# Performance work log

Hardware: AMD Instinct MI355X
Metric: run time of the kernel (lower is better)

Reference implementation:

```python
import jax, jax.numpy as jnp
import numpy as np
import math

B, S, HID = 4, 2048, 2048
H, KV, D = 16, 4, 128  # heads, kv heads, head_dim; n_rep = H//KV = 4
THETA = 1000000.0


def setup_inputs() -> dict:
    key = jax.random.key(0)
    ks = jax.random.split(key, 6)
    x = jax.random.normal(ks[0], (B, S, HID), dtype=jnp.float32)
    # real RoPE tables (theta=1e6), shape [S, D]
    inv_freq = 1.0 / (THETA ** (jnp.arange(0, D, 2, dtype=jnp.float32) / D))
    t = jnp.arange(S, dtype=jnp.float32)
    freqs = jnp.outer(t, inv_freq)                      # [S, D/2]
    emb = jnp.concatenate([freqs, freqs], axis=-1)      # [S, D]
    cos, sin = jnp.cos(emb), jnp.sin(emb)
    scale = 0.02
    wq = jax.random.normal(ks[1], (H * D, HID), dtype=jnp.float32) * scale
    wk = jax.random.normal(ks[2], (KV * D, HID), dtype=jnp.float32) * scale
    wv = jax.random.normal(ks[3], (KV * D, HID), dtype=jnp.float32) * scale
    wo = jax.random.normal(ks[4], (HID, H * D), dtype=jnp.float32) * scale
    return {"x": x, "cos": cos, "sin": sin, "wq": wq, "wk": wk, "wv": wv, "wo": wo}


def _rotate_half(t):
    half = t.shape[-1] // 2
    return jnp.concatenate([-t[..., half:], t[..., :half]], axis=-1)


def reference(x, cos, sin, wq, wk, wv, wo):
    b, s, _ = x.shape
    rep = H // KV
    # QKV projections (torch Linear: y = x @ W^T)
    q = (x @ wq.T).reshape(b, s, H, D)
    k = (x @ wk.T).reshape(b, s, KV, D)
    v = (x @ wv.T).reshape(b, s, KV, D)
    # RoPE, cos/sin broadcast over batch and heads: [1, S, 1, D]
    c = cos[None, :s, None, :]
    si = sin[None, :s, None, :]
    q = q * c + _rotate_half(q) * si
    k = k * c + _rotate_half(k) * si
    # GQA without materializing repeated KV: group q heads as [KV, rep]
    qg = q.reshape(b, s, KV, rep, D)
    scale = 1.0 / math.sqrt(D)
    # flash path in source: SDPA with default is_causal=False -> full (non-causal) attention
    scores = jnp.einsum('bqkrd,bskd->bkrqs', qg, k) * scale  # [B, KV, rep, S, S]
    attn = jax.nn.softmax(scores, axis=-1)
    out = jnp.einsum('bkrqs,bskd->bqkrd', attn, v).reshape(b, s, H * D)
    return out @ wo.T
```

## Files before the change

### kernel.cpp

```cpp
#include <hip/hip_runtime.h>
#include <stdint.h>

#define BB 4
#define SS 2048
#define HIDW 2048
#define NH 16
#define NKV 4
#define DD 128

typedef unsigned short u16;
typedef __attribute__((ext_vector_type(8))) short bf16x8;
typedef __attribute__((ext_vector_type(4))) float f32x4;
typedef __attribute__((ext_vector_type(2))) float f32x2;
typedef __attribute__((ext_vector_type(2))) __bf16 bf16x2;

__device__ __forceinline__ u16 f2bf1(float f) {
  __bf16 h = (__bf16)f;
  return __builtin_bit_cast(u16, h);
}

__device__ __forceinline__ unsigned pkbf(float a, float b) {
  f32x2 v = {a, b};
  bf16x2 h = __builtin_convertvector(v, bf16x2);
  return __builtin_bit_cast(unsigned, h);
}

__device__ __forceinline__ void gld_lds16(const void* g, void* s) {
  __builtin_amdgcn_global_load_lds(
      (const __attribute__((address_space(1))) void*)g,
      (__attribute__((address_space(3))) void*)(unsigned)(uintptr_t)s,
      16, 0, 0);
}

__global__ __launch_bounds__(256) void cast_f32_bf16(const float* __restrict__ in,
                                                     u16* __restrict__ out, int n4) {
  int i = blockIdx.x * 256 + threadIdx.x;
  if (i < n4) {
    float4 f = ((const float4*)in)[i];
    uint2 o;
    o.x = pkbf(f.x, f.y);
    o.y = pkbf(f.z, f.w);
    ((uint2*)out)[i] = o;
  }
}

__global__ __launch_bounds__(256) void gemm_bt(const u16* __restrict__ A,
                                               const u16* __restrict__ Bt,
                                               float* __restrict__ C,
                                               int M, int N, int K) {
  __shared__ u16 As[128 * 32];
  __shared__ u16 Bs[128 * 32];
  const int tid = threadIdx.x;
  const int wave = tid >> 6, lane = tid & 63;
  const int lr = lane & 15, lq = lane >> 4;
  const int row0 = blockIdx.y * 128, col0 = blockIdx.x * 128;
  const int wm = (wave >> 1) * 64, wn = (wave & 1) * 64;

  const int trow = tid >> 2;
  const int tblk = (tid & 3) ^ (trow & 3);
  const u16* aSrc = A + (size_t)(row0 + trow) * K + tblk * 8;
  const u16* bSrc = Bt + (size_t)(col0 + trow) * K + tblk * 8;
  char* ldsA = (char*)As + wave * 1024;
  char* ldsB = (char*)Bs + wave * 1024;

  f32x4 acc[4][4] = {};
  const int aoff = (wm + lr) * 32 + ((lq ^ (lr & 3)) * 8);
  const int boff = (wn + lr) * 32 + ((lq ^ (lr & 3)) * 8);

  for (int k0 = 0; k0 < K; k0 += 32) {
    __syncthreads();
    gld_lds16(aSrc + k0, ldsA);
    gld_lds16(aSrc + (size_t)64 * K + k0, ldsA + 4096);
    gld_lds16(bSrc + k0, ldsB);
    gld_lds16(bSrc + (size_t)64 * K + k0, ldsB + 4096);
    __syncthreads();
    bf16x8 a[4], b[4];
#pragma unroll
    for (int i = 0; i < 4; i++) a[i] = *(const bf16x8*)(As + aoff + i * 512);
#pragma unroll
    for (int j = 0; j < 4; j++) b[j] = *(const bf16x8*)(Bs + boff + j * 512);
#pragma unroll
    for (int i = 0; i < 4; i++)
#pragma unroll
      for (int j = 0; j < 4; j++)
        acc[i][j] = __builtin_amdgcn_mfma_f32_16x16x32_bf16(a[i], b[j], acc[i][j], 0, 0, 0);
  }
#pragma unroll
  for (int i = 0; i < 4; i++) {
    int row = row0 + wm + i * 16 + lq * 4;
#pragma unroll
    for (int j = 0; j < 4; j++) {
      int col = col0 + wn + j * 16 + lr;
      float* cp = C + (size_t)row * N + col;
#pragma unroll
      for (int r = 0; r < 4; r++) cp[(size_t)r * N] = acc[i][j][r];
    }
  }
}

__global__ __launch_bounds__(256) void rope_qk(const float* __restrict__ qkv,
                                               const float* __restrict__ cosT,
                                               const float* __restrict__ sinT,
                                               u16* __restrict__ qb, u16* __restrict__ kb) {
  const float qscale = 0.08838834764831845f;
  int tok = blockIdx.x;
  int b = tok >> 11, s = tok & (SS - 1);
  for (int p = threadIdx.x; p < (NH + NKV) * 64; p += 256) {
    int head = p >> 6, dd = p & 63;
    float c0 = cosT[s * DD + dd];
    float c1 = cosT[s * DD + dd + 64];
    float s0 = sinT[s * DD + dd];
    float s1 = sinT[s * DD + dd + 64];
    if (head < NH) {
      const float* src = qkv + (size_t)tok * 3072 + head * DD;
      float x0 = src[dd], x1 = src[dd + 64];
      u16* dst = qb + ((size_t)(b * NH + head) * SS + s) * DD;
      dst[dd] = f2bf1((x0 * c0 - x1 * s0) * qscale);
      dst[dd + 64] = f2bf1((x1 * c1 + x0 * s1) * qscale);
    } else {
      int kv = head - NH;
      const float* src = qkv + (size_t)tok * 3072 + 2048 + kv * DD;
      float x0 = src[dd], x1 = src[dd + 64];
      u16* dst = kb + ((size_t)(b * NKV + kv) * SS + s) * DD;
      dst[dd] = f2bf1(x0 * c0 - x1 * s0);
      dst[dd + 64] = f2bf1(x1 * c1 + x0 * s1);
    }
  }
}

__global__ __launch_bounds__(256) void v_trans(const float* __restrict__ qkv,
                                               u16* __restrict__ vt) {
  __shared__ float tile[64][65];
  int bk = blockIdx.x;
  int b = bk >> 2, kv = bk & 3;
  int s0 = blockIdx.y * 64, d0 = blockIdx.z * 64;
  int t = threadIdx.x;
  int sl = t >> 2, dc = (t & 3) * 16;
  const float* src = qkv + ((size_t)(b * SS + s0 + sl)) * 3072 + 2560 + kv * DD + d0 + dc;
#pragma unroll
  for (int u = 0; u < 16; u += 4) {
    float4 v4 = *(const float4*)(src + u);
    tile[sl][dc + u] = v4.x; tile[sl][dc + u + 1] = v4.y;
    tile[sl][dc + u + 2] = v4.z; tile[sl][dc + u + 3] = v4.w;
  }
  __syncthreads();
  int dl = t >> 2, sc = (t & 3) * 16;
  u16* dst = vt + ((size_t)bk * DD + d0 + dl) * SS + s0 + sc;
#pragma unroll
  for (int u = 0; u < 16; u++) dst[u] = f2bf1(tile[sc + u][dl]);
}

__global__ __launch_bounds__(256, 2) void flash_attn(const u16* __restrict__ qb,
                                                     const u16* __restrict__ kb,
                                                     const u16* __restrict__ vt,
                                                     u16* __restrict__ ob) {
  __shared__ u16 Ks[64 * 128];
  __shared__ u16 Vs[128 * 64];
  __shared__ u16 Pt[128 * 64];
  const int tid = threadIdx.x;
  const int wave = tid >> 6, lane = tid & 63;
  const int lr = lane & 15, lq = lane >> 4;
  const int q0 = blockIdx.x * 128;
  const int bh = blockIdx.y;
  const int b = bh >> 4, h = bh & 15;
  const int kvh = h >> 2;
  const size_t kbase = (size_t)(b * NKV + kvh) * SS * DD;
  const size_t vbase = (size_t)(b * NKV + kvh) * DD * SS;

  bf16x8 qf[2][4];
#pragma unroll
  for (int nt = 0; nt < 2; nt++) {
    const u16* qrow = qb + ((size_t)bh * SS + q0 + wave * 32 + nt * 16 + lr) * DD + lq * 8;
#pragma unroll
    for (int kk = 0; kk < 4; kk++) qf[nt][kk] = *(const bf16x8*)(qrow + kk * 32);
  }

  f32x4 o_acc[8][2] = {};
  float l_i[2] = {0.0f, 0.0f};

  const int ktrow = tid >> 4;
  const int ktblk = (tid & 15) ^ ktrow;
  const u16* ksrc = kb + kbase + (size_t)ktrow * DD + ktblk * 8;
  const int vtrow = tid >> 3;
  const int vtblk = (tid & 7) ^ (vtrow & 7);
  const u16* vsrc = vt + vbase + (size_t)vtrow * SS + vtblk * 8;
  char* kdst = (char*)Ks + wave * 1024;
  char* vdst = (char*)Vs + wave * 1024;

  for (int s0 = 0; s0 < SS; s0 += 64) {
    __syncthreads();
#pragma unroll
    for (int c = 0; c < 4; c++)
      gld_lds16(ksrc + (size_t)(s0 + c * 16) * DD, kdst + c * 4096);
#pragma unroll
    for (int c = 0; c < 4; c++)
      gld_lds16(vsrc + s0 + (size_t)c * 32 * SS, vdst + c * 4096);
    __syncthreads();

    f32x4 sc[4][2] = {};
#pragma unroll
    for (int kk = 0; kk < 4; kk++) {
#pragma unroll
      for (int mt = 0; mt < 4; mt++) {
        bf16x8 kf = *(const bf16x8*)(Ks + (mt * 16 + lr) * 128 + (((kk * 4 + lq) ^ lr) * 8));
#pragma unroll
        for (int nt = 0; nt < 2; nt++)
          sc[mt][nt] = __builtin_amdgcn_mfma_f32_16x16x32_bf16(kf, qf[nt][kk], sc[mt][nt], 0, 0, 0);
      }
    }

#pragma unroll
    for (int nt = 0; nt < 2; nt++) {
      float rs = 0.0f;
#pragma unroll
      for (int mt = 0; mt < 4; mt++)
#pragma unroll
        for (int r = 0; r < 4; r++) {
          float p = __expf(sc[mt][nt][r]);
          sc[mt][nt][r] = p;
          rs += p;
        }
      l_i[nt] += rs;
      int prow = wave * 32 + nt * 16 + lr;
#pragma unroll
      for (int mt = 0; mt < 4; mt++) {
        uint2 pk;
        pk.x = pkbf(sc[mt][nt][0], sc[mt][nt][1]);
        pk.y = pkbf(sc[mt][nt][2], sc[mt][nt][3]);
        int bb = (mt * 2 + (lq >> 1)) ^ (lr & 7);
        *(uint2*)((char*)Pt + prow * 128 + bb * 16 + (lq & 1) * 8) = pk;
      }
    }

#pragma unroll
    for (int kk2 = 0; kk2 < 2; kk2++) {
      bf16x8 pbf[2];
#pragma unroll
      for (int nt = 0; nt < 2; nt++) {
        int prow = wave * 32 + nt * 16 + lr;
        pbf[nt] = *(const bf16x8*)((char*)Pt + prow * 128 + (((kk2 * 4 + lq) ^ (lr & 7)) * 16));
      }
#pragma unroll
      for (int mt = 0; mt < 8; mt++) {
        bf16x8 vf = *(const bf16x8*)(Vs + (mt * 16 + lr) * 64 + (((kk2 * 4 + lq) ^ (lr & 7)) * 8));
#pragma unroll
        for (int nt = 0; nt < 2; nt++)
          o_acc[mt][nt] = __builtin_amdgcn_mfma_f32_16x16x32_bf16(vf, pbf[nt], o_acc[mt][nt], 0, 0, 0);
      }
    }
  }

#pragma unroll
  for (int nt = 0; nt < 2; nt++) {
    float l = l_i[nt];
    l += __shfl_xor(l, 16, 64);
    l += __shfl_xor(l, 32, 64);
    float inv = 1.0f / l;
    size_t q = (size_t)q0 + wave * 32 + nt * 16 + lr;
    u16* dst = ob + ((size_t)b * SS + q) * HIDW + h * DD + lq * 4;
#pragma unroll
    for (int mt = 0; mt < 8; mt++) {
      uint2 pk;
      pk.x = pkbf(o_acc[mt][nt][0] * inv, o_acc[mt][nt][1] * inv);
      pk.y = pkbf(o_acc[mt][nt][2] * inv, o_acc[mt][nt][3] * inv);
      *(uint2*)(dst + mt * 16) = pk;
    }
  }
}

extern "C" void kernel_launch(void* const* d_in, const int* in_sizes, int n_in,
                              void* d_out, int out_size, void* d_ws, size_t ws_size,
                              hipStream_t stream) {
  const float* x = (const float*)d_in[0];
  const float* cosT = (const float*)d_in[1];
  const float* sinT = (const float*)d_in[2];
  const float* wq = (const float*)d_in[3];
  const float* wk = (const float*)d_in[4];
  const float* wv = (const float*)d_in[5];
  const float* wo = (const float*)d_in[6];
  float* out = (float*)d_out;

  char* ws = (char*)d_ws;
  size_t off = 0;
  auto alloc = [&](size_t bytes) {
    char* p = ws + off;
    off += (bytes + 255) & ~(size_t)255;
    return p;
  };
  const int M = BB * SS;
  u16* xb = (u16*)alloc((size_t)M * HIDW * 2);
  u16* wqkvb = (u16*)alloc((size_t)3072 * HIDW * 2);
  u16* wob = (u16*)alloc((size_t)HIDW * NH * DD * 2);
  float* qkvf = (float*)alloc((size_t)M * 3072 * 4);
  u16* qb = (u16*)alloc((size_t)BB * NH * SS * DD * 2);
  u16* kb = (u16*)alloc((size_t)BB * NKV * SS * DD * 2);
  u16* vt = (u16*)alloc((size_t)BB * NKV * DD * SS * 2);
  u16* ob = (u16*)(void*)qkvf;

  cast_f32_bf16<<<(M * HIDW) / 1024, 256, 0, stream>>>(x, xb, (M * HIDW) / 4);
  cast_f32_bf16<<<(2048 * HIDW) / 1024, 256, 0, stream>>>(wq, wqkvb, (2048 * HIDW) / 4);
  cast_f32_bf16<<<(512 * HIDW) / 1024, 256, 0, stream>>>(wk, wqkvb + (size_t)2048 * HIDW,
                                                         (512 * HIDW) / 4);
  cast_f32_bf16<<<(512 * HIDW) / 1024, 256, 0, stream>>>(wv, wqkvb + (size_t)2560 * HIDW,
                                                         (512 * HIDW) / 4);
  cast_f32_bf16<<<(HIDW * NH * DD) / 1024, 256, 0, stream>>>(wo, wob, (HIDW * NH * DD) / 4);

  gemm_bt<<<dim3(3072 / 128, M / 128), 256, 0, stream>>>(xb, wqkvb, qkvf, M, 3072, HIDW);

  rope_qk<<<M, 256, 0, stream>>>(qkvf, cosT, sinT, qb, kb);
  v_trans<<<dim3(BB * NKV, SS / 64, DD / 64), 256, 0, stream>>>(qkvf, vt);

  flash_attn<<<dim3(SS / 128, BB * NH), 256, 0, stream>>>(qb, kb, vt, ob);

  gemm_bt<<<dim3(HIDW / 128, M / 128), 256, 0, stream>>>(ob, wob, out, M, HIDW, NH * DD);
}
```

Measured before the change: 568.7 us.

## Emit bf16 QKV, widen K/V tiles in attention, and remap blocks per XCD

The QKV projection now writes bf16 instead of fp32, which halves the intermediate traffic read by rope_qk and v_trans; v_trans is rewritten to move bf16 with vector loads and stores. The flash attention kernel loads 128 keys per barrier pair into two LDS buffers, halving the number of synchronisations. It also remaps block indices so blocks sharing the same KV head land on the same XCD, for better L2 reuse. Costs are one extra bf16 rounding of Q/K/V before RoPE and doubled LDS for K/V, which may reduce occupancy.

```diff
diff --git a/kernel.cpp b/kernel.cpp
--- a/kernel.cpp
+++ b/kernel.cpp
@@ -9,6 +9,8 @@
 #define DD 128
 
 typedef unsigned short u16;
+typedef unsigned long long u64;
+typedef unsigned int uint;
 typedef __attribute__((ext_vector_type(8))) short bf16x8;
 typedef __attribute__((ext_vector_type(4))) float f32x4;
 typedef __attribute__((ext_vector_type(2))) float f32x2;
@@ -19,10 +21,14 @@
   return __builtin_bit_cast(u16, h);
 }
 
-__device__ __forceinline__ unsigned pkbf(float a, float b) {
+__device__ __forceinline__ float bf2f(u16 v) {
+  return __uint_as_float((uint)v << 16);
+}
+
+__device__ __forceinline__ uint pkbf(float a, float b) {
   f32x2 v = {a, b};
   bf16x2 h = __builtin_convertvector(v, bf16x2);
-  return __builtin_bit_cast(unsigned, h);
+  return __builtin_bit_cast(uint, h);
 }
 
 __device__ __forceinline__ void gld_lds16(const void* g, void* s) {
@@ -98,7 +104,61 @@
   }
 }
 
-__global__ __launch_bounds__(256) void rope_qk(const float* __restrict__ qkv,
+__global__ __launch_bounds__(256) void gemm_bt_bf16(const u16* __restrict__ A,
+                                                    const u16* __restrict__ Bt,
+                                                    u16* __restrict__ C,
+                                                    int M, int N, int K) {
+  __shared__ u16 As[128 * 32];
+  __shared__ u16 Bs[128 * 32];
+  const int tid = threadIdx.x;
+  const int wave = tid >> 6, lane = tid & 63;
+  const int lr = lane & 15, lq = lane >> 4;
+  const int row0 = blockIdx.y * 128, col0 = blockIdx.x * 128;
+  const int wm = (wave >> 1) * 64, wn = (wave & 1) * 64;
+
+  const int trow = tid >> 2;
+  const int tblk = (tid & 3) ^ (trow & 3);
+  const u16* aSrc = A + (size_t)(row0 + trow) * K + tblk * 8;
+  const u16* bSrc = Bt + (size_t)(col0 + trow) * K + tblk * 8;
+  char* ldsA = (char*)As + wave * 1024;
+  char* ldsB = (char*)Bs + wave * 1024;
+
+  f32x4 acc[4][4] = {};
+  const int aoff = (wm + lr) * 32 + ((lq ^ (lr & 3)) * 8);
+  const int boff = (wn + lr) * 32 + ((lq ^ (lr & 3)) * 8);
+
+  for (int k0 = 0; k0 < K; k0 += 32) {
+    __syncthreads();
+    gld_lds16(aSrc + k0, ldsA);
+    gld_lds16(aSrc + (size_t)64 * K + k0, ldsA + 4096);
+    gld_lds16(bSrc + k0, ldsB);
+    gld_lds16(bSrc + (size_t)64 * K + k0, ldsB + 4096);
+    __syncthreads();
+    bf16x8 a[4], b[4];
+#pragma unroll
+    for (int i = 0; i < 4; i++) a[i] = *(const bf16x8*)(As + aoff + i * 512);
+#pragma unroll
+    for (int j = 0; j < 4; j++) b[j] = *(const bf16x8*)(Bs + boff + j * 512);
+#pragma unroll
+    for (int i = 0; i < 4; i++)
+#pragma unroll
+      for (int j = 0; j < 4; j++)
+        acc[i][j] = __builtin_amdgcn_mfma_f32_16x16x32_bf16(a[i], b[j], acc[i][j], 0, 0, 0);
+  }
+#pragma unroll
+  for (int i = 0; i < 4; i++) {
+    int row = row0 + wm + i * 16 + lq * 4;
+#pragma unroll
+    for (int j = 0; j < 4; j++) {
+      int col = col0 + wn + j * 16 + lr;
+      u16* cp = C + (size_t)row * N + col;
+#pragma unroll
+      for (int r = 0; r < 4; r++) cp[(size_t)r * N] = f2bf1(acc[i][j][r]);
+    }
+  }
+}
+
+__global__ __launch_bounds__(256) void rope_qk(const u16* __restrict__ qkv,
                                                const float* __restrict__ cosT,
                                                const float* __restrict__ sinT,
                                                u16* __restrict__ qb, u16* __restrict__ kb) {
@@ -112,15 +172,15 @@
     float s0 = sinT[s * DD + dd];
     float s1 = sinT[s * DD + dd + 64];
     if (head < NH) {
-      const float* src = qkv + (size_t)tok * 3072 + head * DD;
-      float x0 = src[dd], x1 = src[dd + 64];
+      const u16* src = qkv + (size_t)tok * 3072 + head * DD;
+      float x0 = bf2f(src[dd]), x1 = bf2f(src[dd + 64]);
       u16* dst = qb + ((size_t)(b * NH + head) * SS + s) * DD;
       dst[dd] = f2bf1((x0 * c0 - x1 * s0) * qscale);
       dst[dd + 64] = f2bf1((x1 * c1 + x0 * s1) * qscale);
     } else {
       int kv = head - NH;
-      const float* src = qkv + (size_t)tok * 3072 + 2048 + kv * DD;
-      float x0 = src[dd], x1 = src[dd + 64];
+      const u16* src = qkv + (size_t)tok * 3072 + 2048 + kv * DD;
+      float x0 = bf2f(src[dd]), x1 = bf2f(src[dd + 64]);
       u16* dst = kb + ((size_t)(b * NKV + kv) * SS + s) * DD;
       dst[dd] = f2bf1(x0 * c0 - x1 * s0);
       dst[dd + 64] = f2bf1(x1 * c1 + x0 * s1);
@@ -128,42 +188,57 @@
   }
 }
 
-__global__ __launch_bounds__(256) void v_trans(const float* __restrict__ qkv,
+__global__ __launch_bounds__(256) void v_trans(const u16* __restrict__ qkv,
                                                u16* __restrict__ vt) {
-  __shared__ float tile[64][65];
+  __shared__ u16 tile[64][66];
   int bk = blockIdx.x;
   int b = bk >> 2, kv = bk & 3;
   int s0 = blockIdx.y * 64, d0 = blockIdx.z * 64;
   int t = threadIdx.x;
   int sl = t >> 2, dc = (t & 3) * 16;
-  const float* src = qkv + ((size_t)(b * SS + s0 + sl)) * 3072 + 2560 + kv * DD + d0 + dc;
-#pragma unroll
-  for (int u = 0; u < 16; u += 4) {
-    float4 v4 = *(const float4*)(src + u);
-    tile[sl][dc + u] = v4.x; tile[sl][dc + u + 1] = v4.y;
-    tile[sl][dc + u + 2] = v4.z; tile[sl][dc + u + 3] = v4.w;
-  }
+  const u16* src = qkv + ((size_t)(b * SS + s0 + sl)) * 3072 + 2560 + kv * DD + d0 + dc;
+  uint4 a0 = *(const uint4*)src;
+  uint4 a1 = *(const uint4*)(src + 8);
+  uint* lrow = (uint*)&tile[sl][dc];
+  lrow[0] = a0.x; lrow[1] = a0.y; lrow[2] = a0.z; lrow[3] = a0.w;
+  lrow[4] = a1.x; lrow[5] = a1.y; lrow[6] = a1.z; lrow[7] = a1.w;
   __syncthreads();
   int dl = t >> 2, sc = (t & 3) * 16;
   u16* dst = vt + ((size_t)bk * DD + d0 + dl) * SS + s0 + sc;
-#pragma unroll
-  for (int u = 0; u < 16; u++) dst[u] = f2bf1(tile[sc + u][dl]);
+  uint4 o0, o1;
+  o0.x = (uint)tile[sc + 0][dl] | ((uint)tile[sc + 1][dl] << 16);
+  o0.y = (uint)tile[sc + 2][dl] | ((uint)tile[sc + 3][dl] << 16);
+  o0.z = (uint)tile[sc + 4][dl] | ((uint)tile[sc + 5][dl] << 16);
+  o0.w = (uint)tile[sc + 6][dl] | ((uint)tile[sc + 7][dl] << 16);
+  o1.x = (uint)tile[sc + 8][dl] | ((uint)tile[sc + 9][dl] << 16);
+  o1.y = (uint)tile[sc + 10][dl] | ((uint)tile[sc + 11][dl] << 16);
+  o1.z = (uint)tile[sc + 12][dl] | ((uint)tile[sc + 13][dl] << 16);
+  o1.w = (uint)tile[sc + 14][dl] | ((uint)tile[sc + 15][dl] << 16);
+  *(uint4*)dst = o0;
+  *(uint4*)(dst + 8) = o1;
 }
 
 __global__ __launch_bounds__(256, 2) void flash_attn(const u16* __restrict__ qb,
                                                      const u16* __restrict__ kb,
                                                      const u16* __restrict__ vt,
                                                      u16* __restrict__ ob) {
-  __shared__ u16 Ks[64 * 128];
-  __shared__ u16 Vs[128 * 64];
+  __shared__ u16 Ks[2][64 * 128];
+  __shared__ u16 Vs[2][128 * 64];
   __shared__ u16 Pt[128 * 64];
   const int tid = threadIdx.x;
   const int wave = tid >> 6, lane = tid & 63;
   const int lr = lane & 15, lq = lane >> 4;
-  const int q0 = blockIdx.x * 128;
-  const int bh = blockIdx.y;
-  const int b = bh >> 4, h = bh & 15;
-  const int kvh = h >> 2;
+
+  const int lin = blockIdx.y * 16 + blockIdx.x;
+  const int xcd = lin & 7;
+  const int slot = lin >> 3;
+  const int pr = xcd + ((slot & 1) << 3);
+  const int b = pr >> 2, kvh = pr & 3;
+  const int rest = slot >> 1;
+  const int h = kvh * 4 + (rest & 3);
+  const int q0 = (rest >> 2) * 128;
+  const int bh = b * 16 + h;
+
   const size_t kbase = (size_t)(b * NKV + kvh) * SS * DD;
   const size_t vbase = (size_t)(b * NKV + kvh) * DD * SS;
 
@@ -184,68 +259,77 @@
   const int vtrow = tid >> 3;
   const int vtblk = (tid & 7) ^ (vtrow & 7);
   const u16* vsrc = vt + vbase + (size_t)vtrow * SS + vtblk * 8;
-  char* kdst = (char*)Ks + wave * 1024;
-  char* vdst = (char*)Vs + wave * 1024;
-
-  for (int s0 = 0; s0 < SS; s0 += 64) {
-    __syncthreads();
-#pragma unroll
-    for (int c = 0; c < 4; c++)
-      gld_lds16(ksrc + (size_t)(s0 + c * 16) * DD, kdst + c * 4096);
-#pragma unroll
-    for (int c = 0; c < 4; c++)
-      gld_lds16(vsrc + s0 + (size_t)c * 32 * SS, vdst + c * 4096);
-    __syncthreads();
-
-    f32x4 sc[4][2] = {};
-#pragma unroll
-    for (int kk = 0; kk < 4; kk++) {
-#pragma unroll
-      for (int mt = 0; mt < 4; mt++) {
-        bf16x8 kf = *(const bf16x8*)(Ks + (mt * 16 + lr) * 128 + (((kk * 4 + lq) ^ lr) * 8));
-#pragma unroll
-        for (int nt = 0; nt < 2; nt++)
-          sc[mt][nt] = __builtin_amdgcn_mfma_f32_16x16x32_bf16(kf, qf[nt][kk], sc[mt][nt], 0, 0, 0);
+
+  for (int s0 = 0; s0 < SS; s0 += 128) {
+    __syncthreads();
+#pragma unroll
+    for (int hb = 0; hb < 2; hb++) {
+      const u16* kS = ksrc + (size_t)(s0 + hb * 64) * DD;
+      const u16* vS = vsrc + s0 + hb * 64;
+      char* kd = (char*)(Ks[hb]) + wave * 1024;
+      char* vd = (char*)(Vs[hb]) + wave * 1024;
+#pragma unroll
+      for (int c = 0; c < 4; c++) {
+        gld_lds16(kS + (size_t)c * 16 * DD, kd + c * 4096);
+        gld_lds16(vS + (size_t)c * 32 * SS, vd + c * 4096);
       }
     }
-
-#pragma unroll
-    for (int nt = 0; nt < 2; nt++) {
-      float rs = 0.0f;
-#pragma unroll
-      for (int mt = 0; mt < 4; mt++)
-#pragma unroll
-        for (int r = 0; r < 4; r++) {
-          float p = __expf(sc[mt][nt][r]);
-          sc[mt][nt][r] = p;
-          rs += p;
+    __syncthreads();
+
+#pragma unroll
+    for (int hb = 0; hb < 2; hb++) {
+      const u16* K = Ks[hb];
+      const u16* V = Vs[hb];
+
+      f32x4 sc[4][2] = {};
+#pragma unroll
+      for (int kk = 0; kk < 4; kk++) {
+#pragma unroll
+        for (int mt = 0; mt < 4; mt++) {
+          bf16x8 kf = *(const bf16x8*)(K + (mt * 16 + lr) * 128 + (((kk * 4 + lq) ^ lr) * 8));
+#pragma unroll
+          for (int nt = 0; nt < 2; nt++)
+            sc[mt][nt] = __builtin_amdgcn_mfma_f32_16x16x32_bf16(kf, qf[nt][kk], sc[mt][nt], 0, 0, 0);
         }
-      l_i[nt] += rs;
-      int prow = wave * 32 + nt * 16 + lr;
-#pragma unroll
-      for (int mt = 0; mt < 4; mt++) {
-        uint2 pk;
-        pk.x = pkbf(sc[mt][nt][0], sc[mt][nt][1]);
-        pk.y = pkbf(sc[mt][nt][2], sc[mt][nt][3]);
-        int bb = (mt * 2 + (lq >> 1)) ^ (lr & 7);
-        *(uint2*)((char*)Pt + prow * 128 + bb * 16 + (lq & 1) * 8) = pk;
       }
-    }
-
-#pragma unroll
-    for (int kk2 = 0; kk2 < 2; kk2++) {
-      bf16x8 pbf[2];
+
 #pragma unroll
       for (int nt = 0; nt < 2; nt++) {
+        float rs = 0.0f;
+#pragma unroll
+        for (int mt = 0; mt < 4; mt++)
+#pragma unroll
+          for (int r = 0; r < 4; r++) {
+            float p = __expf(sc[mt][nt][r]);
+            sc[mt][nt][r] = p;
+            rs += p;
+          }
+        l_i[nt] += rs;
         int prow = wave * 32 + nt * 16 + lr;
-        pbf[nt] = *(const bf16x8*)((char*)Pt + prow * 128 + (((kk2 * 4 + lq) ^ (lr & 7)) * 16));
+#pragma unroll
+        for (int mt = 0; mt < 4; mt++) {
+          u64 pw = (u64)pkbf(sc[mt][nt][0], sc[mt][nt][1]) |
+                   ((u64)pkbf(sc[mt][nt][2], sc[mt][nt][3]) << 32);
+          int bb = (mt * 2 + (lq >> 1)) ^ (lr & 7);
+          *(u64*)((char*)Pt + prow * 128 + bb * 16 + (lq & 1) * 8) = pw;
+        }
       }
-#pragma unroll
-      for (int mt = 0; mt < 8; mt++) {
-        bf16x8 vf = *(const bf16x8*)(Vs + (mt * 16 + lr) * 64 + (((kk2 * 4 + lq) ^ (lr & 7)) * 8));
-#pragma unroll
-        for (int nt = 0; nt < 2; nt++)
-          o_acc[mt][nt] = __builtin_amdgcn_mfma_f32_16x16x32_bf16(vf, pbf[nt], o_acc[mt][nt], 0, 0, 0);
+
+#pragma unroll
+      for (int kk2 = 0; kk2 < 2; kk2++) {
+        bf16x8 pbf[2];
+#pragma unroll
+        for (int nt = 0; nt < 2; nt++) {
+          int prow = wave * 32 + nt * 16 + lr;
+          pbf[nt] = *(const bf16x8*)((char*)Pt + prow * 128 + (((kk2 * 4 + lq) ^ (lr & 7)) * 16));
+        }
+#pragma unroll
+        for (int mt = 0; mt < 8; mt++) {
+          bf16x8 vf = *(const bf16x8*)(V + (mt * 16 + lr) * 64 + (((kk2 * 4 + lq) ^ (lr & 7)) * 8));
+#pragma unroll
+          for (int nt = 0; nt < 2; nt++)
+            o_acc[mt][nt] = __builtin_amdgcn_mfma_f32_16x16x32_bf16(vf, pbf[nt], o_acc[mt][nt], 0, 0, 0);
+        }
       }
     }
   }
@@ -291,11 +375,11 @@
   u16* xb = (u16*)alloc((size_t)M * HIDW * 2);
   u16* wqkvb = (u16*)alloc((size_t)3072 * HIDW * 2);
   u16* wob = (u16*)alloc((size_t)HIDW * NH * DD * 2);
-  float* qkvf = (float*)alloc((size_t)M * 3072 * 4);
+  u16* qkvb = (u16*)alloc((size_t)M * 3072 * 2);
   u16* qb = (u16*)alloc((size_t)BB * NH * SS * DD * 2);
   u16* kb = (u16*)alloc((size_t)BB * NKV * SS * DD * 2);
   u16* vt = (u16*)alloc((size_t)BB * NKV * DD * SS * 2);
-  u16* ob = (u16*)(void*)qkvf;
+  u16* ob = qkvb;
 
   cast_f32_bf16<<<(M * HIDW) / 1024, 256, 0, stream>>>(x, xb, (M * HIDW) / 4);
   cast_f32_bf16<<<(2048 * HIDW) / 1024, 256, 0, stream>>>(wq, wqkvb, (2048 * HIDW) / 4);
@@ -305,10 +389,10 @@
                                                          (512 * HIDW) / 4);
   cast_f32_bf16<<<(HIDW * NH * DD) / 1024, 256, 0, stream>>>(wo, wob, (HIDW * NH * DD) / 4);
 
-  gemm_bt<<<dim3(3072 / 128, M / 128), 256, 0, stream>>>(xb, wqkvb, qkvf, M, 3072, HIDW);
-
-  rope_qk<<<M, 256, 0, stream>>>(qkvf, cosT, sinT, qb, kb);
-  v_trans<<<dim3(BB * NKV, SS / 64, DD / 64), 256, 0, stream>>>(qkvf, vt);
+  gemm_bt_bf16<<<dim3(3072 / 128, M / 128), 256, 0, stream>>>(xb, wqkvb, qkvb, M, 3072, HIDW);
+
+  rope_qk<<<M, 256, 0, stream>>>(qkvb, cosT, sinT, qb, kb);
+  v_trans<<<dim3(BB * NKV, SS / 64, DD / 64), 256, 0, stream>>>(qkvb, vt);
 
   flash_attn<<<dim3(SS / 128, BB * NH), 256, 0, stream>>>(qb, kb, vt, ob);
 
```

After: 554.3 us. 1.03x faster.
